# Kernel optimization log

Hardware: AMD Instinct MI355X
Metric: run time of the kernel (lower is better)

Reference implementation:

```python
import jax, jax.numpy as jnp
import numpy as np

WS = 16      # window_size
HEADS = 8    # num_heads


def setup_inputs() -> dict:
    key = jax.random.key(0)
    ks = jax.random.split(key, 3)
    B, C, H, W = 16, 512, 64, 64
    x = jax.random.normal(ks[0], (B, C, H, W), dtype=jnp.float32)
    in_proj_w = jax.random.normal(ks[1], (3 * C, C), dtype=jnp.float32) * 0.02
    in_proj_b = jnp.zeros((3 * C,), dtype=jnp.float32)
    out_w = jax.random.normal(ks[2], (C, C), dtype=jnp.float32) * 0.02
    out_b = jnp.zeros((C,), dtype=jnp.float32)
    return {"x": x, "in_proj_w": in_proj_w, "in_proj_b": in_proj_b,
            "out_w": out_w, "out_b": out_b}


def reference(x, in_proj_w, in_proj_b, out_w, out_b):
    B, C, H, W = x.shape
    pad_h = (-H) % WS
    pad_w = (-W) % WS
    x = jnp.pad(x, ((0, 0), (0, 0), (0, pad_h), (0, pad_w)))
    Hp, Wp = x.shape[2], x.shape[3]
    nH, nW = Hp // WS, Wp // WS
    # window partition: (B,C,Hp,Wp) -> (B*nH*nW, WS*WS, C)
    xw = x.reshape(B, C, nH, WS, nW, WS)
    xw = xw.transpose(0, 2, 4, 3, 5, 1).reshape(B * nH * nW, WS * WS, C)
    # torch MHA default batch_first=False: dim0 = seq (L = B*nH*nW), dim1 = batch (N = WS*WS)
    L, N, _ = xw.shape
    d = C // HEADS
    qkv = xw @ in_proj_w.T + in_proj_b            # (L, N, 3C)
    q, k, v = jnp.split(qkv, 3, axis=-1)
    q = q.reshape(L, N, HEADS, d) * (d ** -0.5)
    k = k.reshape(L, N, HEADS, d)
    v = v.reshape(L, N, HEADS, d)
    scores = jnp.einsum('lnhd,mnhd->nhlm', q, k)  # (N, H, L, L)
    attn = jax.nn.softmax(scores, axis=-1)
    o = jnp.einsum('nhlm,mnhd->lnhd', attn, v).reshape(L, N, C)
    o = o @ out_w.T + out_b                       # (L, N, C)
    # window reverse: -> (B, C, Hp, Wp)
    o = o.reshape(B, nH, nW, WS, WS, C).transpose(0, 5, 1, 3, 2, 4)
    o = o.reshape(B, C, Hp, Wp)
    return o[:, :, :H, :W]
```

## Files before the change

### kernel.cpp

```cpp
#include <hip/hip_runtime.h>
#include <stdint.h>
#include <stddef.h>
#include <math.h>


typedef __bf16 bf16;
typedef __attribute__((ext_vector_type(8))) __bf16 bf16x8;
typedef __attribute__((ext_vector_type(4))) __bf16 bf16x4;
typedef __attribute__((ext_vector_type(4))) float f32x4;

#define MFMA16(A, B, C) __builtin_amdgcn_mfma_f32_16x16x32_bf16((A), (B), (C), 0, 0, 0)

__device__ __forceinline__ float fast_exp2(float x) { return __builtin_amdgcn_exp2f(x); }

__device__ __forceinline__ int aswz(int n, int c) {
  int g = (c >> 3) ^ ((n >> 4) & 7) ^ (n & 7);
  return n * 512 + (g << 3) + (c & 7);
}

__global__ void cvt_weights(const float* __restrict__ w1f, const float* __restrict__ w2f,
                            bf16* __restrict__ w1b, bf16* __restrict__ w2b) {
  int i = (blockIdx.x * blockDim.x + threadIdx.x) * 4;
  const float* s;
  bf16* d;
  int off;
  if (i < 786432) { s = w1f; d = w1b; off = i; }
  else            { s = w2f; d = w2b; off = i - 786432; }
  float4 f = *(const float4*)(s + off);
  bf16x4 r;
  r[0] = (bf16)f.x; r[1] = (bf16)f.y; r[2] = (bf16)f.z; r[3] = (bf16)f.w;
  *(bf16x4*)(d + off) = r;
}

__global__ void __launch_bounds__(256, 2) gemm_qkv(
    const float* __restrict__ x, const bf16* __restrict__ w1,
    const float* __restrict__ b1,
    bf16* __restrict__ qo, bf16* __restrict__ ko, bf16* __restrict__ vo) {
  extern __shared__ bf16 Al[];
  bf16* Ep = Al + 64 * 512;
  const int tid = threadIdx.x;
  const int bm  = blockIdx.x;
  const int l   = bm >> 2;
  const int n0  = (bm & 3) << 6;
  const int b   = l >> 4, ih = (l >> 2) & 3, iw = l & 3;
  const int h0  = ih * 16 + (n0 >> 4);
  const int w0  = iw * 16;

  for (int j = 0; j < 32; ++j) {
    int f4  = j * 256 + tid;
    int c   = f4 >> 4;
    int qq  = f4 & 15;
    int wsh = qq >> 2;
    int w4  = (qq & 3) << 2;
    float4 xf = *(const float4*)(x + (((b * 512 + c) * 64 + h0 + wsh) * 64 + w0 + w4));
    int nb = wsh * 16 + w4;
    Al[aswz(nb + 0, c)] = (bf16)xf.x;
    Al[aswz(nb + 1, c)] = (bf16)xf.y;
    Al[aswz(nb + 2, c)] = (bf16)xf.z;
    Al[aswz(nb + 3, c)] = (bf16)xf.w;
  }
  __syncthreads();

  const int wave = tid >> 6, lane = tid & 63;
  const int l15 = lane & 15, quad = lane >> 4;
  const int wc = wave;
  bf16* Epw = Ep + wave * 16 * 72;
  const f32x4 fz = {0.f, 0.f, 0.f, 0.f};

  for (int nc = 0; nc < 6; ++nc) {
    const int t0w = nc * 256 + wc * 64;
    f32x4 acc[4][4];
#pragma unroll
    for (int a = 0; a < 4; ++a)
#pragma unroll
      for (int c2 = 0; c2 < 4; ++c2) acc[a][c2] = fz;

    bf16x8 bfr[4];
#pragma unroll
    for (int ct = 0; ct < 4; ++ct)
      bfr[ct] = *(const bf16x8*)&w1[(size_t)(t0w + ct * 16 + l15) * 512 + quad * 8];
#pragma unroll
    for (int ks = 0; ks < 16; ++ks) {
      bf16x8 bnx[4];
      if (ks < 15) {
#pragma unroll
        for (int ct = 0; ct < 4; ++ct)
          bnx[ct] = *(const bf16x8*)&w1[(size_t)(t0w + ct * 16 + l15) * 512 + (ks + 1) * 32 + quad * 8];
      }
      bf16x8 af[4];
#pragma unroll
      for (int lt = 0; lt < 4; ++lt)
        af[lt] = *(const bf16x8*)&Al[aswz(lt * 16 + l15, ks * 32 + quad * 8)];
#pragma unroll
      for (int lt = 0; lt < 4; ++lt)
#pragma unroll
        for (int ct = 0; ct < 4; ++ct)
          acc[lt][ct] = MFMA16(af[lt], bfr[ct], acc[lt][ct]);
#pragma unroll
      for (int ct = 0; ct < 4; ++ct) bfr[ct] = bnx[ct];
    }

    const int which = t0w >> 9;
    const int hh = (t0w & 511) >> 6;
    bf16* dst = (which == 0) ? qo : (which == 1) ? ko : vo;
    const float scale = (which == 0) ? 0.125f : 1.0f;
    float bias[4];
#pragma unroll
    for (int ct = 0; ct < 4; ++ct) bias[ct] = b1[t0w + ct * 16 + l15];

#pragma unroll
    for (int lt = 0; lt < 4; ++lt) {
#pragma unroll
      for (int ct = 0; ct < 4; ++ct)
#pragma unroll
        for (int r = 0; r < 4; ++r)
          Epw[(quad * 4 + r) * 72 + ct * 16 + l15] =
              (bf16)((acc[lt][ct][r] + bias[ct]) * scale);
      const int rr = lane >> 3, ch8 = (lane & 7) * 8;
#pragma unroll
      for (int half = 0; half < 2; ++half) {
        int row = half * 8 + rr;
        bf16x8 vv = *(const bf16x8*)&Epw[row * 72 + ch8];
        int n = n0 + lt * 16 + row;
        *(bf16x8*)&dst[((size_t)(n * 8 + hh) * 256 + l) * 64 + ch8] = vv;
      }
    }
  }
}

__global__ void __launch_bounds__(512, 2) attn_win(
    bf16* __restrict__ qio, const bf16* __restrict__ kg, const bf16* __restrict__ vg) {
  extern __shared__ bf16 sm[];
  bf16* Kl = sm;
  bf16* Vt = sm + 256 * 72;
  bf16* Pl = Vt + 64 * 264;
  const int tid = threadIdx.x;
  const int bb = blockIdx.x;
  const int n = bb >> 3, h = bb & 7;
  const size_t base = (size_t)(n * 8 + h) * 16384;
  const bf16* Kg = kg + base;
  const bf16* Vg = vg + base;
  bf16* Qg = qio + base;

  for (int j = 0; j < 4; ++j) {
    int cc = j * 512 + tid;
    int m = cc >> 3, dc = cc & 7;
    bf16x8 t = *(const bf16x8*)(Kg + m * 64 + dc * 8);
    *(bf16x8*)&Kl[m * 72 + dc * 8] = t;
  }
  for (int j = 0; j < 4; ++j) {
    int cc = j * 512 + tid;
    int dc = cc >> 8, m = cc & 255;
    bf16x8 t = *(const bf16x8*)(Vg + m * 64 + dc * 8);
#pragma unroll
    for (int s = 0; s < 8; ++s) Vt[(dc * 8 + s) * 264 + m] = t[s];
  }

  const int wave = tid >> 6, lane = tid & 63;
  const int l15 = lane & 15, quad = lane >> 4;
  const int lb = wave * 32;
  bf16* Pw = Pl + wave * 16 * 264;

  bf16x8 qf[2][2];
#pragma unroll
  for (int lt = 0; lt < 2; ++lt)
#pragma unroll
    for (int ks = 0; ks < 2; ++ks)
      qf[lt][ks] = *(const bf16x8*)(Qg + (lb + lt * 16 + l15) * 64 + ks * 32 + quad * 8);

  __syncthreads();

  const f32x4 fz = {0.f, 0.f, 0.f, 0.f};
  const float LOG2E = 1.44269504088896340736f;
  for (int lt = 0; lt < 2; ++lt) {
    f32x4 s[16];
#pragma unroll
    for (int mt = 0; mt < 16; ++mt) s[mt] = fz;
#pragma unroll
    for (int mt = 0; mt < 16; ++mt)
#pragma unroll
      for (int ks = 0; ks < 2; ++ks) {
        bf16x8 kf = *(const bf16x8*)&Kl[(mt * 16 + l15) * 72 + ks * 32 + quad * 8];
        s[mt] = MFMA16(qf[lt][ks], kf, s[mt]);
      }
    float rmax[4], rsum[4];
#pragma unroll
    for (int r = 0; r < 4; ++r) {
      float mx = s[0][r];
#pragma unroll
      for (int mt = 1; mt < 16; ++mt) mx = fmaxf(mx, s[mt][r]);
#pragma unroll
      for (int xo = 1; xo < 16; xo <<= 1) mx = fmaxf(mx, __shfl_xor(mx, xo, 16));
      rmax[r] = mx;
      rsum[r] = 0.f;
    }
#pragma unroll
    for (int mt = 0; mt < 16; ++mt) {
#pragma unroll
      for (int r = 0; r < 4; ++r) {
        float p = fast_exp2((s[mt][r] - rmax[r]) * LOG2E);
        bf16 pb = (bf16)p;
        rsum[r] += (float)pb;
        Pw[(quad * 4 + r) * 264 + mt * 16 + l15] = pb;
      }
    }
#pragma unroll
    for (int r = 0; r < 4; ++r)
#pragma unroll
      for (int xo = 1; xo < 16; xo <<= 1) rsum[r] += __shfl_xor(rsum[r], xo, 16);

    bf16x8 pf[8];
#pragma unroll
    for (int mk = 0; mk < 8; ++mk)
      pf[mk] = *(const bf16x8*)&Pw[l15 * 264 + mk * 32 + quad * 8];
    f32x4 of[4];
#pragma unroll
    for (int dt = 0; dt < 4; ++dt) of[dt] = fz;
#pragma unroll
    for (int dt = 0; dt < 4; ++dt)
#pragma unroll
      for (int mk = 0; mk < 8; ++mk) {
        bf16x8 vf = *(const bf16x8*)&Vt[(dt * 16 + l15) * 264 + mk * 32 + quad * 8];
        of[dt] = MFMA16(pf[mk], vf, of[dt]);
      }
    float inv[4];
#pragma unroll
    for (int r = 0; r < 4; ++r) inv[r] = 1.0f / rsum[r];

    bf16* Ew = Pw;
#pragma unroll
    for (int dt = 0; dt < 4; ++dt)
#pragma unroll
      for (int r = 0; r < 4; ++r)
        Ew[(quad * 4 + r) * 72 + dt * 16 + l15] = (bf16)(of[dt][r] * inv[r]);
    const int rr = lane >> 3, ch8 = (lane & 7) * 8;
#pragma unroll
    for (int half = 0; half < 2; ++half) {
      int row = half * 8 + rr;
      bf16x8 vv = *(const bf16x8*)&Ew[row * 72 + ch8];
      *(bf16x8*)(Qg + (lb + lt * 16 + row) * 64 + ch8) = vv;
    }
  }
}

__global__ void __launch_bounds__(256, 2) gemm_out(
    const bf16* __restrict__ og, const bf16* __restrict__ w2,
    const float* __restrict__ b2, float* __restrict__ out) {
  extern __shared__ bf16 Al[];
  const int tid = threadIdx.x;
  const int bm = blockIdx.x;
  const int l = bm >> 2;
  const int n0 = (bm & 3) << 6;
  const int b = l >> 4, ih = (l >> 2) & 3, iw = l & 3;

  for (int j = 0; j < 16; ++j) {
    int cc = j * 256 + tid;
    int nl = cc >> 6;
    int ch = cc & 63;
    int hh = ch >> 3, d8 = (ch & 7) * 8;
    bf16x8 t = *(const bf16x8*)(og + ((size_t)((n0 + nl) * 8 + hh) * 256 + l) * 64 + d8);
    *(bf16x8*)&Al[aswz(nl, ch * 8)] = t;
  }
  __syncthreads();

  const int wave = tid >> 6, lane = tid & 63;
  const int l15 = lane & 15, quad = lane >> 4;
  const int wc = wave;
  const f32x4 fz = {0.f, 0.f, 0.f, 0.f};

  for (int nc = 0; nc < 2; ++nc) {
    const int t0w = nc * 256 + wc * 64;
    f32x4 acc[4][4];
#pragma unroll
    for (int a = 0; a < 4; ++a)
#pragma unroll
      for (int c2 = 0; c2 < 4; ++c2) acc[a][c2] = fz;

    bf16x8 bfr[4];
#pragma unroll
    for (int ct = 0; ct < 4; ++ct)
      bfr[ct] = *(const bf16x8*)&w2[(size_t)(t0w + ct * 16 + l15) * 512 + quad * 8];
#pragma unroll
    for (int ks = 0; ks < 16; ++ks) {
      bf16x8 bnx[4];
      if (ks < 15) {
#pragma unroll
        for (int ct = 0; ct < 4; ++ct)
          bnx[ct] = *(const bf16x8*)&w2[(size_t)(t0w + ct * 16 + l15) * 512 + (ks + 1) * 32 + quad * 8];
      }
      bf16x8 af[4];
#pragma unroll
      for (int lt = 0; lt < 4; ++lt)
        af[lt] = *(const bf16x8*)&Al[aswz(lt * 16 + l15, ks * 32 + quad * 8)];
#pragma unroll
      for (int lt = 0; lt < 4; ++lt)
#pragma unroll
        for (int ct = 0; ct < 4; ++ct)
          acc[lt][ct] = MFMA16(bfr[ct], af[lt], acc[lt][ct]);
#pragma unroll
      for (int ct = 0; ct < 4; ++ct) bfr[ct] = bnx[ct];
    }

#pragma unroll
    for (int ct = 0; ct < 4; ++ct) {
      float4 bias4 = *(const float4*)&b2[t0w + ct * 16 + quad * 4];
#pragma unroll
      for (int lt = 0; lt < 4; ++lt) {
        const int nbase = n0 + lt * 16;
        const int wsh = nbase >> 4;
        size_t rowbase = (((size_t)b * 512) * 64 + (size_t)ih * 16 + wsh) * 64 + iw * 16 + l15;
#pragma unroll
        for (int r = 0; r < 4; ++r) {
          int cout = t0w + ct * 16 + quad * 4 + r;
          out[rowbase + (size_t)cout * 4096] = acc[lt][ct][r] + ((const float*)&bias4)[r];
        }
      }
    }
  }
}

extern "C" void kernel_launch(void* const* d_in, const int* in_sizes, int n_in,
                              void* d_out, int out_size, void* d_ws, size_t ws_size,
                              hipStream_t stream) {
  (void)in_sizes; (void)n_in; (void)out_size; (void)ws_size;
  const float* x   = (const float*)d_in[0];
  const float* w1f = (const float*)d_in[1];
  const float* b1  = (const float*)d_in[2];
  const float* w2f = (const float*)d_in[3];
  const float* b2  = (const float*)d_in[4];
  float* out = (float*)d_out;

  char* ws = (char*)d_ws;
  bf16* q   = (bf16*)(ws);
  bf16* k   = (bf16*)(ws + 67108864ull);
  bf16* v   = (bf16*)(ws + 134217728ull);
  bf16* w1b = (bf16*)(ws + 201326592ull);
  bf16* w2b = (bf16*)(ws + 201326592ull + 1572864ull);

  const int LDS_QKV  = (64 * 512 + 4 * 16 * 72) * 2;
  const int LDS_ATTN = (256 * 72 + 64 * 264 + 8 * 16 * 264) * 2;
  const int LDS_OUT  = 64 * 512 * 2;
  hipFuncSetAttribute(reinterpret_cast<const void*>(gemm_qkv),
                      hipFuncAttributeMaxDynamicSharedMemorySize, LDS_QKV);
  hipFuncSetAttribute(reinterpret_cast<const void*>(attn_win),
                      hipFuncAttributeMaxDynamicSharedMemorySize, LDS_ATTN);
  hipFuncSetAttribute(reinterpret_cast<const void*>(gemm_out),
                      hipFuncAttributeMaxDynamicSharedMemorySize, LDS_OUT);

  hipLaunchKernelGGL(cvt_weights, dim3(1024), dim3(256), 0, stream, w1f, w2f, w1b, w2b);
  hipLaunchKernelGGL(gemm_qkv, dim3(1024), dim3(256), LDS_QKV, stream, x, w1b, b1, q, k, v);
  hipLaunchKernelGGL(attn_win, dim3(2048), dim3(512), LDS_ATTN, stream, q, k, v);
  hipLaunchKernelGGL(gemm_out, dim3(1024), dim3(256), LDS_OUT, stream, q, w2b, b2, out);
}
```

Before: 666.9 us.

## Pre-pack weights into MFMA fragment order and widen GEMM blocks to 8 waves

New measurement: 1.263 ms. 89.3% more time.

```diff
diff --git a/kernel.cpp b/kernel.cpp
--- a/kernel.cpp
+++ b/kernel.cpp
@@ -18,26 +18,31 @@
   return n * 512 + (g << 3) + (c & 7);
 }
 
-__global__ void cvt_weights(const float* __restrict__ w1f, const float* __restrict__ w2f,
-                            bf16* __restrict__ w1b, bf16* __restrict__ w2b) {
-  int i = (blockIdx.x * blockDim.x + threadIdx.x) * 4;
-  const float* s;
-  bf16* d;
-  int off;
-  if (i < 786432) { s = w1f; d = w1b; off = i; }
-  else            { s = w2f; d = w2b; off = i - 786432; }
-  float4 f = *(const float4*)(s + off);
-  bf16x4 r;
-  r[0] = (bf16)f.x; r[1] = (bf16)f.y; r[2] = (bf16)f.z; r[3] = (bf16)f.w;
-  *(bf16x4*)(d + off) = r;
-}
-
-__global__ void __launch_bounds__(256, 2) gemm_qkv(
-    const float* __restrict__ x, const bf16* __restrict__ w1,
+__global__ void cvt_pack(const float* __restrict__ w1f, const float* __restrict__ w2f,
+                         bf16* __restrict__ w1p, bf16* __restrict__ w2p) {
+  int i = blockIdx.x * 256 + threadIdx.x;
+  const float* src;
+  bf16* dst;
+  if (i < 98304) { src = w1f; dst = w1p; }
+  else           { src = w2f; dst = w2p; i -= 98304; }
+  int lane = i & 63;
+  int ks   = (i >> 6) & 15;
+  int t    = i >> 10;
+  int cout = t * 16 + (lane & 15);
+  int c0   = ks * 32 + (lane >> 4) * 8;
+  float4 a = *(const float4*)(src + (size_t)cout * 512 + c0);
+  float4 b = *(const float4*)(src + (size_t)cout * 512 + c0 + 4);
+  bf16x8 r;
+  r[0] = (bf16)a.x; r[1] = (bf16)a.y; r[2] = (bf16)a.z; r[3] = (bf16)a.w;
+  r[4] = (bf16)b.x; r[5] = (bf16)b.y; r[6] = (bf16)b.z; r[7] = (bf16)b.w;
+  *(bf16x8*)(dst + (size_t)i * 8) = r;
+}
+
+__global__ void __launch_bounds__(512, 4) gemm_qkv(
+    const float* __restrict__ x, const bf16* __restrict__ w1p,
     const float* __restrict__ b1,
     bf16* __restrict__ qo, bf16* __restrict__ ko, bf16* __restrict__ vo) {
   extern __shared__ bf16 Al[];
-  bf16* Ep = Al + 64 * 512;
   const int tid = threadIdx.x;
   const int bm  = blockIdx.x;
   const int l   = bm >> 2;
@@ -46,8 +51,8 @@
   const int h0  = ih * 16 + (n0 >> 4);
   const int w0  = iw * 16;
 
-  for (int j = 0; j < 32; ++j) {
-    int f4  = j * 256 + tid;
+  for (int j = 0; j < 16; ++j) {
+    int f4  = j * 512 + tid;
     int c   = f4 >> 4;
     int qq  = f4 & 15;
     int wsh = qq >> 2;
@@ -63,30 +68,23 @@
 
   const int wave = tid >> 6, lane = tid & 63;
   const int l15 = lane & 15, quad = lane >> 4;
-  const int wc = wave;
-  bf16* Epw = Ep + wave * 16 * 72;
   const f32x4 fz = {0.f, 0.f, 0.f, 0.f};
 
-  for (int nc = 0; nc < 6; ++nc) {
-    const int t0w = nc * 256 + wc * 64;
+  for (int nc = 0; nc < 3; ++nc) {
+    const int t0w = nc * 512 + wave * 64;
+    const int tb  = t0w >> 4;
     f32x4 acc[4][4];
 #pragma unroll
     for (int a = 0; a < 4; ++a)
 #pragma unroll
       for (int c2 = 0; c2 < 4; ++c2) acc[a][c2] = fz;
 
-    bf16x8 bfr[4];
-#pragma unroll
-    for (int ct = 0; ct < 4; ++ct)
-      bfr[ct] = *(const bf16x8*)&w1[(size_t)(t0w + ct * 16 + l15) * 512 + quad * 8];
 #pragma unroll
     for (int ks = 0; ks < 16; ++ks) {
-      bf16x8 bnx[4];
-      if (ks < 15) {
-#pragma unroll
-        for (int ct = 0; ct < 4; ++ct)
-          bnx[ct] = *(const bf16x8*)&w1[(size_t)(t0w + ct * 16 + l15) * 512 + (ks + 1) * 32 + quad * 8];
-      }
+      bf16x8 bfr[4];
+#pragma unroll
+      for (int ct = 0; ct < 4; ++ct)
+        bfr[ct] = *(const bf16x8*)&w1p[((size_t)((tb + ct) * 16 + ks) * 64 + lane) * 8];
       bf16x8 af[4];
 #pragma unroll
       for (int lt = 0; lt < 4; ++lt)
@@ -96,35 +94,25 @@
 #pragma unroll
         for (int ct = 0; ct < 4; ++ct)
           acc[lt][ct] = MFMA16(af[lt], bfr[ct], acc[lt][ct]);
-#pragma unroll
-      for (int ct = 0; ct < 4; ++ct) bfr[ct] = bnx[ct];
-    }
-
-    const int which = t0w >> 9;
-    const int hh = (t0w & 511) >> 6;
-    bf16* dst = (which == 0) ? qo : (which == 1) ? ko : vo;
-    const float scale = (which == 0) ? 0.125f : 1.0f;
+    }
+
+    bf16* dst = (nc == 0) ? qo : (nc == 1) ? ko : vo;
+    const float scale = (nc == 0) ? 0.125f : 1.0f;
+    const int hh = wave;
     float bias[4];
 #pragma unroll
     for (int ct = 0; ct < 4; ++ct) bias[ct] = b1[t0w + ct * 16 + l15];
 
 #pragma unroll
-    for (int lt = 0; lt < 4; ++lt) {
+    for (int lt = 0; lt < 4; ++lt)
 #pragma unroll
       for (int ct = 0; ct < 4; ++ct)
 #pragma unroll
-        for (int r = 0; r < 4; ++r)
-          Epw[(quad * 4 + r) * 72 + ct * 16 + l15] =
+        for (int r = 0; r < 4; ++r) {
+          int n = n0 + lt * 16 + quad * 4 + r;
+          dst[((size_t)(n * 8 + hh) * 256 + l) * 64 + ct * 16 + l15] =
               (bf16)((acc[lt][ct][r] + bias[ct]) * scale);
-      const int rr = lane >> 3, ch8 = (lane & 7) * 8;
-#pragma unroll
-      for (int half = 0; half < 2; ++half) {
-        int row = half * 8 + rr;
-        bf16x8 vv = *(const bf16x8*)&Epw[row * 72 + ch8];
-        int n = n0 + lt * 16 + row;
-        *(bf16x8*)&dst[((size_t)(n * 8 + hh) * 256 + l) * 64 + ch8] = vv;
-      }
-    }
+        }
   }
 }
 
@@ -243,8 +231,8 @@
   }
 }
 
-__global__ void __launch_bounds__(256, 2) gemm_out(
-    const bf16* __restrict__ og, const bf16* __restrict__ w2,
+__global__ void __launch_bounds__(512, 4) gemm_out(
+    const bf16* __restrict__ og, const bf16* __restrict__ w2p,
     const float* __restrict__ b2, float* __restrict__ out) {
   extern __shared__ bf16 Al[];
   const int tid = threadIdx.x;
@@ -253,8 +241,8 @@
   const int n0 = (bm & 3) << 6;
   const int b = l >> 4, ih = (l >> 2) & 3, iw = l & 3;
 
-  for (int j = 0; j < 16; ++j) {
-    int cc = j * 256 + tid;
+  for (int j = 0; j < 8; ++j) {
+    int cc = j * 512 + tid;
     int nl = cc >> 6;
     int ch = cc & 63;
     int hh = ch >> 3, d8 = (ch & 7) * 8;
@@ -265,55 +253,45 @@
 
   const int wave = tid >> 6, lane = tid & 63;
   const int l15 = lane & 15, quad = lane >> 4;
-  const int wc = wave;
+  const int t0w = wave * 64;
+  const int tb  = wave * 4;
   const f32x4 fz = {0.f, 0.f, 0.f, 0.f};
 
-  for (int nc = 0; nc < 2; ++nc) {
-    const int t0w = nc * 256 + wc * 64;
-    f32x4 acc[4][4];
-#pragma unroll
-    for (int a = 0; a < 4; ++a)
-#pragma unroll
-      for (int c2 = 0; c2 < 4; ++c2) acc[a][c2] = fz;
-
+  f32x4 acc[4][4];
+#pragma unroll
+  for (int a = 0; a < 4; ++a)
+#pragma unroll
+    for (int c2 = 0; c2 < 4; ++c2) acc[a][c2] = fz;
+
+#pragma unroll
+  for (int ks = 0; ks < 16; ++ks) {
     bf16x8 bfr[4];
 #pragma unroll
     for (int ct = 0; ct < 4; ++ct)
-      bfr[ct] = *(const bf16x8*)&w2[(size_t)(t0w + ct * 16 + l15) * 512 + quad * 8];
-#pragma unroll
-    for (int ks = 0; ks < 16; ++ks) {
-      bf16x8 bnx[4];
-      if (ks < 15) {
-#pragma unroll
-        for (int ct = 0; ct < 4; ++ct)
-          bnx[ct] = *(const bf16x8*)&w2[(size_t)(t0w + ct * 16 + l15) * 512 + (ks + 1) * 32 + quad * 8];
-      }
-      bf16x8 af[4];
-#pragma unroll
-      for (int lt = 0; lt < 4; ++lt)
-        af[lt] = *(const bf16x8*)&Al[aswz(lt * 16 + l15, ks * 32 + quad * 8)];
-#pragma unroll
-      for (int lt = 0; lt < 4; ++lt)
-#pragma unroll
-        for (int ct = 0; ct < 4; ++ct)
-          acc[lt][ct] = MFMA16(bfr[ct], af[lt], acc[lt][ct]);
-#pragma unroll
-      for (int ct = 0; ct < 4; ++ct) bfr[ct] = bnx[ct];
-    }
-
-#pragma unroll
-    for (int ct = 0; ct < 4; ++ct) {
-      float4 bias4 = *(const float4*)&b2[t0w + ct * 16 + quad * 4];
-#pragma unroll
-      for (int lt = 0; lt < 4; ++lt) {
-        const int nbase = n0 + lt * 16;
-        const int wsh = nbase >> 4;
-        size_t rowbase = (((size_t)b * 512) * 64 + (size_t)ih * 16 + wsh) * 64 + iw * 16 + l15;
-#pragma unroll
-        for (int r = 0; r < 4; ++r) {
-          int cout = t0w + ct * 16 + quad * 4 + r;
-          out[rowbase + (size_t)cout * 4096] = acc[lt][ct][r] + ((const float*)&bias4)[r];
-        }
+      bfr[ct] = *(const bf16x8*)&w2p[((size_t)((tb + ct) * 16 + ks) * 64 + lane) * 8];
+    bf16x8 af[4];
+#pragma unroll
+    for (int lt = 0; lt < 4; ++lt)
+      af[lt] = *(const bf16x8*)&Al[aswz(lt * 16 + l15, ks * 32 + quad * 8)];
+#pragma unroll
+    for (int lt = 0; lt < 4; ++lt)
+#pragma unroll
+      for (int ct = 0; ct < 4; ++ct)
+        acc[lt][ct] = MFMA16(bfr[ct], af[lt], acc[lt][ct]);
+  }
+
+#pragma unroll
+  for (int ct = 0; ct < 4; ++ct) {
+    float4 bias4 = *(const float4*)&b2[t0w + ct * 16 + quad * 4];
+#pragma unroll
+    for (int lt = 0; lt < 4; ++lt) {
+      const int nbase = n0 + lt * 16;
+      const int wsh = nbase >> 4;
+      size_t rowbase = (((size_t)b * 512) * 64 + (size_t)ih * 16 + wsh) * 64 + iw * 16 + l15;
+#pragma unroll
+      for (int r = 0; r < 4; ++r) {
+        int cout = t0w + ct * 16 + quad * 4 + r;
+        out[rowbase + (size_t)cout * 4096] = acc[lt][ct][r] + ((const float*)&bias4)[r];
       }
     }
   }
@@ -334,10 +312,10 @@
   bf16* q   = (bf16*)(ws);
   bf16* k   = (bf16*)(ws + 67108864ull);
   bf16* v   = (bf16*)(ws + 134217728ull);
-  bf16* w1b = (bf16*)(ws + 201326592ull);
-  bf16* w2b = (bf16*)(ws + 201326592ull + 1572864ull);
-
-  const int LDS_QKV  = (64 * 512 + 4 * 16 * 72) * 2;
+  bf16* w1p = (bf16*)(ws + 201326592ull);
+  bf16* w2p = (bf16*)(ws + 201326592ull + 1572864ull);
+
+  const int LDS_QKV  = 64 * 512 * 2;
   const int LDS_ATTN = (256 * 72 + 64 * 264 + 8 * 16 * 264) * 2;
   const int LDS_OUT  = 64 * 512 * 2;
   hipFuncSetAttribute(reinterpret_cast<const void*>(gemm_qkv),
@@ -347,8 +325,8 @@
   hipFuncSetAttribute(reinterpret_cast<const void*>(gemm_out),
                       hipFuncAttributeMaxDynamicSharedMemorySize, LDS_OUT);
 
-  hipLaunchKernelGGL(cvt_weights, dim3(1024), dim3(256), 0, stream, w1f, w2f, w1b, w2b);
-  hipLaunchKernelGGL(gemm_qkv, dim3(1024), dim3(256), LDS_QKV, stream, x, w1b, b1, q, k, v);
+  hipLaunchKernelGGL(cvt_pack, dim3(512), dim3(256), 0, stream, w1f, w2f, w1p, w2p);
+  hipLaunchKernelGGL(gemm_qkv, dim3(1024), dim3(512), LDS_QKV, stream, x, w1p, b1, q, k, v);
   hipLaunchKernelGGL(attn_win, dim3(2048), dim3(512), LDS_ATTN, stream, q, k, v);
-  hipLaunchKernelGGL(gemm_out, dim3(1024), dim3(256), LDS_OUT, stream, q, w2b, b2, out);
-}
+  hipLaunchKernelGGL(gemm_out, dim3(1024), dim3(512), LDS_OUT, stream, q, w2p, b2, out);
+}
```
